# Kernel optimization log

Measured on AMD Instinct MI355X. Metric: run time of the kernel, lower is better.

The kernel has to match this reference:

```python
import jax, jax.numpy as jnp
import numpy as np

D_MODEL = 512; D_STATE = 64; D_CONV = 4; HEADDIM = 64
D_INNER = 2 * D_MODEL              # expand=2
NHEADS = D_INNER // HEADDIM        # 16
CONV_DIM = D_INNER + 2 * D_STATE   # 1152
D_IN_PROJ = 2 * D_INNER + 2 * D_STATE + NHEADS  # 2192
BATCH, SEQ = 4, 1024
EPS = 1e-5


def rmsnorm(x, w):
    return x * jax.lax.rsqrt(jnp.mean(x * x, axis=-1, keepdims=True) + EPS) * w


def mamba2(u, in_w, conv_w, conv_b, dt_bias, A_log, D, gnorm_w, out_w):
    b, l, _ = u.shape
    zxbcdt = u @ in_w.T                                  # [b,l,D_IN_PROJ]
    z = zxbcdt[..., :D_INNER]
    xBC = zxbcdt[..., D_INNER:D_INNER + CONV_DIM]
    dt = jax.nn.softplus(zxbcdt[..., -NHEADS:] + dt_bias)  # [b,l,h]
    # causal depthwise conv1d (kernel D_CONV, left pad) + silu
    pad = jnp.pad(xBC, ((0, 0), (D_CONV - 1, 0), (0, 0)))
    acc = conv_b
    for k in range(D_CONV):
        acc = acc + pad[:, k:k + l, :] * conv_w[:, k]
    xBC = jax.nn.silu(acc)
    x = xBC[..., :D_INNER].reshape(b, l, NHEADS, HEADDIM)
    Bm = xBC[..., D_INNER:D_INNER + D_STATE]             # [b,l,n]
    Cm = xBC[..., D_INNER + D_STATE:]                    # [b,l,n]
    A = -jnp.exp(A_log)                                  # [h]
    decay = jnp.exp(dt * A)                              # [b,l,h]
    dtx = dt[..., None] * x                              # [b,l,h,p]

    def step(h, inp):
        dec, dx, Bt, Ct = inp
        h = h * dec[:, :, None, None] + dx[..., None] * Bt[:, None, None, :]
        y = jnp.einsum('bhpn,bn->bhp', h, Ct)
        return h, y

    h0 = jnp.zeros((b, NHEADS, HEADDIM, D_STATE), u.dtype)
    _, ys = jax.lax.scan(step, h0, (decay.transpose(1, 0, 2),
                                    dtx.transpose(1, 0, 2, 3),
                                    Bm.transpose(1, 0, 2),
                                    Cm.transpose(1, 0, 2)))
    y = ys.transpose(1, 0, 2, 3) + x * D[None, None, :, None]  # [b,l,h,p]
    y = y.reshape(b, l, D_INNER)
    y = rmsnorm(y * jax.nn.silu(z), gnorm_w)             # gated RMSNorm
    return y @ out_w.T


def setup_inputs() -> dict:
    key = jax.random.key(0)
    ks = iter(jax.random.split(key, 32))
    def rn(shape, scale=0.02):
        return jax.random.normal(next(ks), shape, dtype=jnp.float32) * scale
    inp = {
        'x': jax.random.normal(next(ks), (BATCH, SEQ, D_MODEL), dtype=jnp.float32),
        'norm_w': jnp.ones((D_MODEL,), jnp.float32),
    }
    for p in ('f', 'b'):
        inp[p + '_in_w'] = rn((D_IN_PROJ, D_MODEL))
        inp[p + '_conv_w'] = rn((CONV_DIM, D_CONV), 0.1)
        inp[p + '_conv_b'] = jnp.zeros((CONV_DIM,), jnp.float32)
        inp[p + '_dt_bias'] = rn((NHEADS,), 0.5)
        inp[p + '_A_log'] = jnp.log(jnp.arange(1, NHEADS + 1, dtype=jnp.float32))
        inp[p + '_D'] = jnp.ones((NHEADS,), jnp.float32)
        inp[p + '_gnorm_w'] = jnp.ones((D_INNER,), jnp.float32)
        inp[p + '_out_w'] = rn((D_MODEL, D_INNER))
    inp['proj_w'] = rn((D_MODEL, 2 * D_MODEL))
    return inp


def reference(x, norm_w,
              f_in_w, f_conv_w, f_conv_b, f_dt_bias, f_A_log, f_D, f_gnorm_w, f_out_w,
              b_in_w, b_conv_w, b_conv_b, b_dt_bias, b_A_log, b_D, b_gnorm_w, b_out_w,
              proj_w):
    h = rmsnorm(x, norm_w)
    fo = mamba2(h, f_in_w, f_conv_w, f_conv_b, f_dt_bias, f_A_log, f_D, f_gnorm_w, f_out_w)
    bo = jnp.flip(mamba2(jnp.flip(h, 1), b_in_w, b_conv_w, b_conv_b, b_dt_bias,
                         b_A_log, b_D, b_gnorm_w, b_out_w), 1)
    return x + jnp.concatenate([fo, bo], axis=-1) @ proj_w.T
```

## Files before the change

### kernel.cpp

```cpp
#include <hip/hip_runtime.h>
#include <math.h>

typedef unsigned short u16;
typedef __bf16  bf16x8 __attribute__((ext_vector_type(8)));
typedef float   f32x4  __attribute__((ext_vector_type(4)));
typedef unsigned short u16x8 __attribute__((ext_vector_type(8)));

#define SEQ 1024
#define MR  4096
#define DIP 2192
#define DI  1024
#define NH  16
#define CD  1152
#define NCH 32
#define CT  32
#define NIN (DIP*512)
#define NOUT (512*1024)
#define ZROW 4384

__device__ __forceinline__ u16 f2bf(float f) {
  union { float f; unsigned u; } v; v.f = f;
  unsigned r = v.u + 0x7FFFu + ((v.u >> 16) & 1u);
  return (u16)(r >> 16);
}
__device__ __forceinline__ float bf2f(u16 h) {
  union { unsigned u; float f; } v; v.u = ((unsigned)h) << 16; return v.f;
}
__device__ __forceinline__ void splitbf(float v, u16& h, u16& l) {
  h = f2bf(v); l = f2bf(v - bf2f(h));
}
__device__ __forceinline__ float sigm(float x){ return 1.f/(1.f+__expf(-x)); }

__device__ __forceinline__ unsigned packbf(float v) {
  u16 hh, ll; splitbf(v, hh, ll);
  return (unsigned)hh | ((unsigned)ll << 16);
}
__device__ __forceinline__ float unpackf(unsigned w) {
  return bf2f((u16)w) + bf2f((u16)(w >> 16));
}

__device__ __forceinline__ void unpack8(const unsigned* p, bf16x8& H, bf16x8& L) {
  uint4 a = *(const uint4*)p, b = *(const uint4*)(p+4);
  u16x8 hu, lu;
  hu[0]=(u16)a.x; lu[0]=(u16)(a.x>>16);
  hu[1]=(u16)a.y; lu[1]=(u16)(a.y>>16);
  hu[2]=(u16)a.z; lu[2]=(u16)(a.z>>16);
  hu[3]=(u16)a.w; lu[3]=(u16)(a.w>>16);
  hu[4]=(u16)b.x; lu[4]=(u16)(b.x>>16);
  hu[5]=(u16)b.y; lu[5]=(u16)(b.y>>16);
  hu[6]=(u16)b.z; lu[6]=(u16)(b.z>>16);
  hu[7]=(u16)b.w; lu[7]=(u16)(b.w>>16);
  H = __builtin_bit_cast(bf16x8, hu);
  L = __builtin_bit_cast(bf16x8, lu);
}
__device__ __forceinline__ void unpack8s(const unsigned* p, int stride, bf16x8& H, bf16x8& L) {
  u16x8 hu, lu;
  #pragma unroll
  for (int jj=0;jj<8;jj++){ unsigned w = p[(size_t)jj*stride]; hu[jj]=(u16)w; lu[jj]=(u16)(w>>16); }
  H = __builtin_bit_cast(bf16x8, hu);
  L = __builtin_bit_cast(bf16x8, lu);
}

__device__ __forceinline__ void gl16(const u16* g, u16* l) {
  __builtin_amdgcn_global_load_lds((const __attribute__((address_space(1))) void*)g,
                                   (__attribute__((address_space(3))) void*)l,
                                   16, 0, 0);
}

__global__ __launch_bounds__(256) void prep(
  const float* __restrict__ x, const float* __restrict__ norm_w,
  const float* __restrict__ f_in, const float* __restrict__ b_in,
  const float* __restrict__ f_out, const float* __restrict__ b_out,
  const float* __restrict__ proj,
  u16* __restrict__ H, u16* __restrict__ L, unsigned* __restrict__ wpk,
  u16* __restrict__ hbh, u16* __restrict__ hbl)
{
  int blk = blockIdx.x, tid = threadIdx.x;
  if (blk < MR) {
    int m = blk;
    const float* xr = x + (size_t)m*512;
    float2 v = *(const float2*)&xr[tid*2];
    float ss = v.x*v.x + v.y*v.y;
    #pragma unroll
    for (int off=32; off; off>>=1) ss += __shfl_xor(ss, off, 64);
    __shared__ float red[4];
    if ((tid&63)==0) red[tid>>6] = ss;
    __syncthreads();
    float total = red[0]+red[1]+red[2]+red[3];
    float rs = rsqrtf(total*(1.f/512.f) + 1e-5f);
    float2 w2 = *(const float2*)&norm_w[tid*2];
    u16 h0,l0,h1,l1;
    splitbf(v.x*rs*w2.x, h0, l0);
    splitbf(v.y*rs*w2.y, h1, l1);
    *(unsigned*)&hbh[(size_t)m*512 + tid*2] = (unsigned)h0 | ((unsigned)h1<<16);
    *(unsigned*)&hbl[(size_t)m*512 + tid*2] = (unsigned)l0 | ((unsigned)l1<<16);
  } else {
    int i = (blk - MR)*256 + tid;
    constexpr int TOT = 2*NIN + 3*NOUT;
    if (i >= TOT) return;
    float v;
    if (i < NIN)               v = f_in[i];
    else if (i < 2*NIN)        v = b_in[i-NIN];
    else if (i < 2*NIN+NOUT)   v = f_out[i-2*NIN];
    else if (i < 2*NIN+2*NOUT) v = b_out[i-2*NIN-NOUT];
    else                       v = proj[i-2*NIN-2*NOUT];
    if (i < 2*NIN) {
      u16 hh, ll; splitbf(v, hh, ll);
      H[i] = hh; L[i] = ll;
    } else {
      wpk[i - 2*NIN] = packbf(v);
    }
  }
}

__global__ __launch_bounds__(256) void gemm_in(
    const u16* __restrict__ Ah, const u16* __restrict__ Al,
    const u16* __restrict__ Wh, const u16* __restrict__ Wl,
    float* __restrict__ C0,
    const unsigned* __restrict__ wpk,
    u16* __restrict__ Wch, u16* __restrict__ Wcl)
{
  constexpr int K = 512;
  constexpr int N = DIP;
  __shared__ __align__(16) u16 sAh[128*32];
  __shared__ __align__(16) u16 sAl[128*32];
  __shared__ __align__(16) u16 sBh[128*32];
  __shared__ __align__(16) u16 sBl[128*32];
  const int tid = threadIdx.x;
  if (blockIdx.y >= 18) {
    int widx = (blockIdx.y - 18)*64 + blockIdx.x*2 + blockIdx.z;
    int d = widx & 1;
    int p0 = ((widx>>1)&7)*128;
    int o0 = (widx>>4)*64;
    int wv = tid>>6, lane = tid&63;
    int quad = lane>>4, l16 = lane&15;
    const unsigned* owp = wpk + (size_t)d*NOUT;
    const unsigned* pjp = wpk + 2*(size_t)NOUT;
    int pc = p0 + wv*32;
    f32x4 acc[4][2] = {};
    for (int kt=0; kt<512; kt+=32) {
      bf16x8 ahf[4], alf[4], bhf[2], blf[2];
      #pragma unroll
      for (int ia=0; ia<4; ia++)
        unpack8(pjp + (size_t)(o0 + 16*ia + l16)*1024 + d*512 + kt + quad*8, ahf[ia], alf[ia]);
      #pragma unroll
      for (int jb=0; jb<2; jb++)
        unpack8s(owp + (size_t)(kt + quad*8)*1024 + pc + 16*jb + l16, 1024, bhf[jb], blf[jb]);
      #pragma unroll
      for (int ia=0; ia<4; ia++)
        #pragma unroll
        for (int jb=0; jb<2; jb++) {
          f32x4 t = __builtin_amdgcn_mfma_f32_16x16x32_bf16(ahf[ia], blf[jb], acc[ia][jb], 0,0,0);
          t       = __builtin_amdgcn_mfma_f32_16x16x32_bf16(alf[ia], bhf[jb], t,           0,0,0);
          acc[ia][jb] = __builtin_amdgcn_mfma_f32_16x16x32_bf16(ahf[ia], bhf[jb], t,       0,0,0);
        }
    }
    #pragma unroll
    for (int ia=0; ia<4; ia++)
    #pragma unroll
    for (int jb=0; jb<2; jb++)
    #pragma unroll
    for (int r=0; r<4; r++) {
      int o = o0 + 16*ia + quad*4 + r;
      int p = pc + 16*jb + l16;
      u16 hh, ll; splitbf(acc[ia][jb][r], hh, ll);
      Wch[(size_t)d*NOUT + (size_t)o*1024 + p] = hh;
      Wcl[(size_t)d*NOUT + (size_t)o*1024 + p] = ll;
    }
    return;
  }
  const int dir = blockIdx.z;
  const int m0 = blockIdx.x * 128;
  const int n0 = blockIdx.y * 128;
  const int lane = tid & 63;
  const int wid  = tid >> 6;
  const u16* wh_p = Wh + (size_t)dir*NIN;
  const u16* wl_p = Wl + (size_t)dir*NIN;
  const int j0 = wid, j1 = wid + 4;
  const int cp = lane & 3;
  auto goff = [&](int j, bool isB)->size_t {
    int row = 16*j + (lane>>2);
    int s = (row>>1) & 3;
    int kc = (cp ^ s) * 8;
    int grow;
    if (!isB) {
      grow = m0 + row;
      if (dir) grow = (grow & ~1023) + (1023 - (grow & 1023));
    } else {
      grow = n0 + row;
      if (grow >= N) grow = N-1;
    }
    return (size_t)grow*K + kc;
  };
  const size_t a0 = goff(j0,false), a1 = goff(j1,false);
  const size_t b0 = goff(j0,true),  b1 = goff(j1,true);
  const int wm = (wid & 1) * 64;
  const int wn = (wid >> 1) * 64;
  const int quad = lane >> 4;
  const int l16  = lane & 15;
  const int qx = quad ^ ((l16>>1)&3);
  const int baseA = ((wm + l16)*4 + qx)*8;
  const int baseB = ((wn + l16)*4 + qx)*8;
  f32x4 acc[4][4] = {};
  for (int kt = 0; kt < K; kt += 32) {
    __syncthreads();
    gl16(Ah + a0 + kt, &sAh[j0*512]);  gl16(Ah + a1 + kt, &sAh[j1*512]);
    gl16(Al + a0 + kt, &sAl[j0*512]);  gl16(Al + a1 + kt, &sAl[j1*512]);
    gl16(wh_p + b0 + kt, &sBh[j0*512]);  gl16(wh_p + b1 + kt, &sBh[j1*512]);
    gl16(wl_p + b0 + kt, &sBl[j0*512]);  gl16(wl_p + b1 + kt, &sBl[j1*512]);
    __syncthreads();
    bf16x8 ah[4], al[4], bh[4], bl[4];
    #pragma unroll
    for (int i=0;i<4;i++) {
      ah[i] = *(const bf16x8*)&sAh[baseA + i*512];
      al[i] = *(const bf16x8*)&sAl[baseA + i*512];
    }
    #pragma unroll
    for (int j=0;j<4;j++) {
      bh[j] = *(const bf16x8*)&sBh[baseB + j*512];
      bl[j] = *(const bf16x8*)&sBl[baseB + j*512];
    }
    #pragma unroll
    for (int i=0;i<4;i++)
      #pragma unroll
      for (int j=0;j<4;j++) {
        f32x4 t = __builtin_amdgcn_mfma_f32_16x16x32_bf16(ah[i], bl[j], acc[i][j], 0,0,0);
        t       = __builtin_amdgcn_mfma_f32_16x16x32_bf16(al[i], bh[j], t,         0,0,0);
        acc[i][j] = __builtin_amdgcn_mfma_f32_16x16x32_bf16(ah[i], bh[j], t,       0,0,0);
      }
  }
  #pragma unroll
  for (int i=0;i<4;i++)
  #pragma unroll
  for (int j=0;j<4;j++)
  #pragma unroll
  for (int r=0;r<4;r++) {
    int mo = m0 + wm + i*16 + quad*4 + r;
    int no = n0 + wn + j*16 + l16;
    if (no < N) C0[((size_t)dir*MR + mo)*DIP + no] = acc[i][j][r];
  }
}

__global__ __launch_bounds__(256) void gemm_final(
    const u16* __restrict__ zt, const u16* __restrict__ Wch, const u16* __restrict__ Wcl,
    const float* __restrict__ X0, float* __restrict__ out, float* __restrict__ Pb)
{
  constexpr int K = 1024;
  __shared__ __align__(16) u16 sAh[64*32];
  __shared__ __align__(16) u16 sAl[64*32];
  __shared__ __align__(16) u16 sBh[128*32];
  __shared__ __align__(16) u16 sBl[128*32];
  const int tid = threadIdx.x;
  const int dir = blockIdx.z;
  const int m0 = blockIdx.x * 64;
  const int n0 = blockIdx.y * 128;
  const int lane = tid & 63;
  const int wid  = tid >> 6;
  const u16* ah_p = zt + 2048 + (size_t)dir*MR*ZROW;
  const u16* al_p = zt + 3072 + (size_t)dir*MR*ZROW;
  const u16* wh_p = Wch + (size_t)dir*NOUT;
  const u16* wl_p = Wcl + (size_t)dir*NOUT;
  const int cp = lane & 3;
  auto goffA = [&](int j)->size_t {
    int row = 16*j + (lane>>2);
    int s = (row>>1) & 3;
    int kc = (cp ^ s) * 8;
    int grow = m0 + row;
    if (dir) grow = (grow & ~1023) + (1023 - (grow & 1023));
    return (size_t)grow*ZROW + kc;
  };
  auto goffB = [&](int j)->size_t {
    int row = 16*j + (lane>>2);
    int s = (row>>1) & 3;
    int kc = (cp ^ s) * 8;
    return (size_t)(n0 + row)*1024 + kc;
  };
  const size_t a0 = goffA(wid);
  const size_t b0 = goffB(wid), b1 = goffB(wid+4);
  const int quad = lane >> 4;
  const int l16  = lane & 15;
  const int qx = quad ^ ((l16>>1)&3);
  const int baseA = (l16*4 + qx)*8;
  const int baseB = ((wid*32 + l16)*4 + qx)*8;
  f32x4 acc[4][2] = {};
  for (int kt = 0; kt < K; kt += 32) {
    __syncthreads();
    gl16(ah_p + a0 + kt, &sAh[wid*512]);
    gl16(al_p + a0 + kt, &sAl[wid*512]);
    gl16(wh_p + b0 + kt, &sBh[wid*512]);  gl16(wh_p + b1 + kt, &sBh[(wid+4)*512]);
    gl16(wl_p + b0 + kt, &sBl[wid*512]);  gl16(wl_p + b1 + kt, &sBl[(wid+4)*512]);
    __syncthreads();
    bf16x8 ah[4], al[4], bh[2], bl[2];
    #pragma unroll
    for (int i=0;i<4;i++) {
      ah[i] = *(const bf16x8*)&sAh[baseA + i*512];
      al[i] = *(const bf16x8*)&sAl[baseA + i*512];
    }
    #pragma unroll
    for (int j=0;j<2;j++) {
      bh[j] = *(const bf16x8*)&sBh[baseB + j*512];
      bl[j] = *(const bf16x8*)&sBl[baseB + j*512];
    }
    #pragma unroll
    for (int i=0;i<4;i++)
      #pragma unroll
      for (int j=0;j<2;j++) {
        f32x4 t = __builtin_amdgcn_mfma_f32_16x16x32_bf16(ah[i], bl[j], acc[i][j], 0,0,0);
        t       = __builtin_amdgcn_mfma_f32_16x16x32_bf16(al[i], bh[j], t,         0,0,0);
        acc[i][j] = __builtin_amdgcn_mfma_f32_16x16x32_bf16(ah[i], bh[j], t,       0,0,0);
      }
  }
  #pragma unroll
  for (int i=0;i<4;i++)
  #pragma unroll
  for (int j=0;j<2;j++)
  #pragma unroll
  for (int r=0;r<4;r++) {
    int mo = m0 + i*16 + quad*4 + r;
    int no = n0 + wid*32 + j*16 + l16;
    float v = acc[i][j][r];
    if (dir == 0) out[(size_t)mo*512 + no] = v + X0[(size_t)mo*512 + no];
    else          Pb[(size_t)mo*512 + no] = v;
  }
}

__global__ __launch_bounds__(256) void addout(float* __restrict__ out,
                                              const float* __restrict__ Pb)
{
  size_t i = ((size_t)blockIdx.x*256 + threadIdx.x)*4;
  float4 a = *(const float4*)&out[i];
  float4 b = *(const float4*)&Pb[i];
  a.x += b.x; a.y += b.y; a.z += b.z; a.w += b.w;
  *(float4*)&out[i] = a;
}

__global__ __launch_bounds__(320) void conv_dt(
  const float* __restrict__ Z,
  const float* __restrict__ f_cw, const float* __restrict__ f_cb,
  const float* __restrict__ b_cw, const float* __restrict__ b_cb,
  const float* __restrict__ f_dtb, const float* __restrict__ b_dtb,
  unsigned* __restrict__ xconv,
  unsigned* __restrict__ Bc, unsigned* __restrict__ Cc,
  float* __restrict__ dtq)
{
  int bsw = blockIdx.x;
  int b = (bsw & 7)*256 + (bsw >> 3);
  int r0 = b*4;
  int dir = r0 >> 12;
  int t0 = r0 & 1023;
  const float* cw  = dir ? b_cw : f_cw;
  const float* cb  = dir ? b_cb : f_cb;
  const float* dtb = dir ? b_dtb : f_dtb;
  int tid = threadIdx.x;
  if (tid < 288) {
    int c0 = tid*4;
    float4 w0 = *(const float4*)&cw[c0*4];
    float4 w1 = *(const float4*)&cw[(c0+1)*4];
    float4 w2 = *(const float4*)&cw[(c0+2)*4];
    float4 w3 = *(const float4*)&cw[(c0+3)*4];
    float4 cb4 = *(const float4*)&cb[c0];
    const float4 zero4 = {0.f,0.f,0.f,0.f};
    float4 wnd[7];
    #pragma unroll
    for (int j=0;j<7;j++) {
      int a = r0 - 3 + j;
      wnd[j] = (a >= 0) ? *(const float4*)(Z + (size_t)a*DIP + 1024 + c0) : zero4;
    }
    #pragma unroll
    for (int k=0;k<4;k++) {
      int t = t0 + k;
      float4 z0 = (t >= 3) ? wnd[k]   : zero4;
      float4 z1 = (t >= 2) ? wnd[k+1] : zero4;
      float4 z2 = (t >= 1) ? wnd[k+2] : zero4;
      float4 z3 = wnd[k+3];
      float4 a = cb4;
      a.x += z0.x*w0.x + z1.x*w0.y + z2.x*w0.z + z3.x*w0.w;
      a.y += z0.y*w1.x + z1.y*w1.y + z2.y*w1.z + z3.y*w1.w;
      a.z += z0.z*w2.x + z1.z*w2.y + z2.z*w2.z + z3.z*w2.w;
      a.w += z0.w*w3.x + z1.w*w3.y + z2.w*w3.z + z3.w*w3.w;
      float4 v;
      v.x = a.x * sigm(a.x); v.y = a.y * sigm(a.y);
      v.z = a.z * sigm(a.z); v.w = a.w * sigm(a.w);
      uint4 pv;
      pv.x = packbf(v.x); pv.y = packbf(v.y);
      pv.z = packbf(v.z); pv.w = packbf(v.w);
      int bm = r0 + k;
      if (c0 < 1024)      *(uint4*)&xconv[(size_t)bm*DI + c0] = pv;
      else if (c0 < 1088) *(uint4*)&Bc[(size_t)bm*64 + (c0-1024)] = pv;
      else                *(uint4*)&Cc[(size_t)bm*64 + (c0-1088)] = pv;
    }
  }
  if (tid < NH) {
    #pragma unroll
    for (int k=0;k<4;k++) {
      int bm = r0 + k;
      float dtraw = Z[(size_t)bm*DIP + 2176 + tid] + dtb[tid];
      float dt = (dtraw > 20.f) ? dtraw : log1pf(__expf(dtraw));
      dtq[(size_t)bm*NH + tid] = dt;
    }
  }
}

__global__ __launch_bounds__(256) void scan_mfma(
  const float* __restrict__ dtq, const unsigned* __restrict__ xconv,
  const unsigned* __restrict__ Bc, const unsigned* __restrict__ Cc,
  const float* __restrict__ f_Al, const float* __restrict__ b_Al,
  float* __restrict__ yraw, float* __restrict__ cumdec, float* __restrict__ S)
{
  __shared__ __align__(16) u16 sMh[4][32*40];
  __shared__ __align__(16) u16 sMl[4][32*40];
  __shared__ float scum[4][32];
  __shared__ float sdt[4][32];
  int bx = blockIdx.x;
  int hq = bx & 3, chunk = (bx>>2)&(NCH-1), dirb = bx>>7;
  int w = threadIdx.x >> 6, lane = threadIdx.x & 63;
  int h = hq*4 + w;
  int base_row = dirb*1024 + chunk*CT;
  const int quad = lane >> 4, l16 = lane & 15;
  const float* Al = (dirb >= 4) ? b_Al : f_Al;
  float A = -__expf(Al[h]);
  float dtl = 0.f, cum = 0.f;
  if (lane < 32) { dtl = dtq[(size_t)(base_row + lane)*16 + h]; cum = dtl; }
  #pragma unroll
  for (int off=1; off<32; off<<=1) {
    int src = (lane >= off) ? lane-off : lane;
    float o = __shfl(cum, src);
    if (lane >= off && lane < 32) cum += o;
  }
  if (lane < 32) {
    sdt[w][lane]  = dtl;
    scum[w][lane] = cum;
    cumdec[(size_t)(base_row + lane)*16 + h] = __expf(A*cum);
  }
  bf16x8 chf[2][2], clf[2][2], bhf[2][2], blf[2][2];
  #pragma unroll
  for (int i=0;i<2;i++)
  #pragma unroll
  for (int kk=0;kk<2;kk++) {
    unpack8(Cc + (size_t)(base_row + 16*i + l16)*64 + kk*32 + quad*8, chf[i][kk], clf[i][kk]);
    unpack8(Bc + (size_t)(base_row + 16*i + l16)*64 + kk*32 + quad*8, bhf[i][kk], blf[i][kk]);
  }
  f32x4 g[2][2];
  __builtin_amdgcn_s_setprio(1);
  #pragma unroll
  for (int i=0;i<2;i++)
  #pragma unroll
  for (int j=0;j<2;j++) {
    f32x4 acc = {};
    #pragma unroll
    for (int kk=0;kk<2;kk++) {
      acc = __builtin_amdgcn_mfma_f32_16x16x32_bf16(chf[i][kk], blf[j][kk], acc, 0,0,0);
      acc = __builtin_amdgcn_mfma_f32_16x16x32_bf16(clf[i][kk], bhf[j][kk], acc, 0,0,0);
      acc = __builtin_amdgcn_mfma_f32_16x16x32_bf16(chf[i][kk], bhf[j][kk], acc, 0,0,0);
    }
    g[i][j] = acc;
  }
  __builtin_amdgcn_s_setprio(0);
  float ctt[2][4];
  #pragma unroll
  for (int i=0;i<2;i++)
  #pragma unroll
  for (int r=0;r<4;r++) ctt[i][r] = scum[w][16*i + quad*4 + r];
  #pragma unroll
  for (int j=0;j<2;j++) {
    int s = 16*j + l16;
    float cts = scum[w][s];
    float dts = sdt[w][s];
    #pragma unroll
    for (int i=0;i<2;i++)
    #pragma unroll
    for (int r=0;r<4;r++) {
      int t = 16*i + quad*4 + r;
      float mv = (s <= t) ? g[i][j][r] * __expf(A*(ctt[i][r]-cts)) * dts : 0.f;
      u16 hh, ll; splitbf(mv, hh, ll);
      sMh[w][t*40 + s] = hh;
      sMl[w][t*40 + s] = ll;
    }
  }
  bf16x8 xhf[4], xlf[4];
  const unsigned* xp = xconv + (size_t)(base_row + quad*8)*1024 + h*64 + l16;
  #pragma unroll
  for (int jp=0;jp<4;jp++) unpack8s(xp + 16*jp, 1024, xhf[jp], xlf[jp]);
  bf16x8 mhf[2], mlf[2];
  #pragma unroll
  for (int i=0;i<2;i++) {
    mhf[i] = *(const bf16x8*)&sMh[w][(16*i + l16)*40 + quad*8];
    mlf[i] = *(const bf16x8*)&sMl[w][(16*i + l16)*40 + quad*8];
  }
  __builtin_amdgcn_s_setprio(1);
  #pragma unroll
  for (int i=0;i<2;i++)
  #pragma unroll
  for (int jp=0;jp<4;jp++) {
    f32x4 acc = {};
    acc = __builtin_amdgcn_mfma_f32_16x16x32_bf16(mhf[i], xlf[jp], acc, 0,0,0);
    acc = __builtin_amdgcn_mfma_f32_16x16x32_bf16(mlf[i], xhf[jp], acc, 0,0,0);
    acc = __builtin_amdgcn_mfma_f32_16x16x32_bf16(mhf[i], xhf[jp], acc, 0,0,0);
    #pragma unroll
    for (int r=0;r<4;r++)
      yraw[(size_t)(base_row + 16*i + quad*4 + r)*1024 + h*64 + 16*jp + l16] = acc[r];
  }
  __builtin_amdgcn_s_setprio(0);
  float wv[8];
  float ct31 = scum[w][31];
  #pragma unroll
  for (int jj=0;jj<8;jj++) {
    int s = quad*8 + jj;
    wv[jj] = sdt[w][s] * __expf(A*(ct31 - scum[w][s]));
  }
  bf16x8 wbh[4], wbl[4];
  #pragma unroll
  for (int j2=0;j2<4;j2++) {
    u16x8 hu, lu; u16 hh, ll;
    #pragma unroll
    for (int jj=0;jj<8;jj++) {
      float b = unpackf(Bc[(size_t)(base_row + quad*8 + jj)*64 + 16*j2 + l16]);
      splitbf(wv[jj]*b, hh, ll); hu[jj]=hh; lu[jj]=ll;
    }
    wbh[j2] = __builtin_bit_cast(bf16x8, hu);
    wbl[j2] = __builtin_bit_cast(bf16x8, lu);
  }
  size_t inst = ((size_t)(dirb*16+h)*NCH + chunk)*4096;
  __builtin_amdgcn_s_setprio(1);
  #pragma unroll
  for (int mp=0;mp<4;mp++)
  #pragma unroll
  for (int j2=0;j2<4;j2++) {
    f32x4 acc = {};
    acc = __builtin_amdgcn_mfma_f32_16x16x32_bf16(xhf[mp], wbl[j2], acc, 0,0,0);
    acc = __builtin_amdgcn_mfma_f32_16x16x32_bf16(xlf[mp], wbh[j2], acc, 0,0,0);
    acc = __builtin_amdgcn_mfma_f32_16x16x32_bf16(xhf[mp], wbh[j2], acc, 0,0,0);
    #pragma unroll
    for (int r=0;r<4;r++)
      S[inst + (size_t)(16*mp + quad*4 + r)*64 + 16*j2 + l16] = acc[r];
  }
  __builtin_amdgcn_s_setprio(0);
}

__global__ __launch_bounds__(256) void scan_comb(
  const float* __restrict__ cumdec, float* __restrict__ S)
{
  int ih = blockIdx.x >> 4;
  int sub = blockIdx.x & 15;
  int dirb = ih >> 4, h = ih & 15;
  int elem = sub*256 + threadIdx.x;
  size_t base = (size_t)ih*NCH*4096 + elem;
  float hr = 0.f;
  #pragma unroll
  for (int c=0;c<NCH;c++) {
    float P = cumdec[((size_t)(dirb*1024 + c*CT + CT-1))*16 + h];
    float s = S[base + c*4096];
    S[base + c*4096] = __builtin_bit_cast(float, packbf(hr));
    hr = fmaf(hr, P, s);
  }
}

__global__ __launch_bounds__(1024) void scan_y2_gate(
  const unsigned* __restrict__ Cc, const float* __restrict__ cumdec,
  const float* __restrict__ S, const float* __restrict__ yraw,
  const unsigned* __restrict__ xconv, const float* Z, u16* zt,
  const float* __restrict__ f_D, const float* __restrict__ b_D,
  const float* __restrict__ f_gw, const float* __restrict__ b_gw)
{
  __shared__ float vbuf[32][1028];
  __shared__ float red[32][17];
  __shared__ float rsb[32];
  int bx = blockIdx.x;
  int chunk = bx & (NCH-1), dirb = bx >> 5;
  int w = threadIdx.x >> 6, lane = threadIdx.x & 63;
  int h = w;
  int dir = dirb >> 2;
  int row0 = dirb*1024 + chunk*CT;
  const int quad = lane>>4, l16 = lane&15;
  const float* Dp  = dir ? b_D  : f_D;
  const float* gwp = dir ? b_gw : f_gw;
  float Dv = Dp[h];

  f32x4 acc[2][4] = {};
  float at[2][4] = {};
  if (chunk > 0) {
    size_t inst = ((size_t)(dirb*16+h)*NCH + chunk)*4096;
    #pragma unroll
    for (int i=0;i<2;i++)
    #pragma unroll
    for (int r=0;r<4;r++)
      at[i][r] = cumdec[(size_t)(row0 + 16*i + quad*4 + r)*16 + h];
    bf16x8 chf[2][2], clf[2][2];
    #pragma unroll
    for (int i=0;i<2;i++)
    #pragma unroll
    for (int kk=0;kk<2;kk++)
      unpack8(Cc + (size_t)(row0 + 16*i + l16)*64 + kk*32 + quad*8, chf[i][kk], clf[i][kk]);
    const unsigned* Sp = (const unsigned*)S;
    __builtin_amdgcn_s_setprio(1);
    #pragma unroll
    for (int j=0;j<4;j++) {
      bf16x8 hhf[2], hlf[2];
      #pragma unroll
      for (int kk=0;kk<2;kk++)
        unpack8(Sp + inst + (size_t)(16*j + l16)*64 + kk*32 + quad*8, hhf[kk], hlf[kk]);
      #pragma unroll
      for (int i=0;i<2;i++) {
        f32x4 a2 = acc[i][j];
        #pragma unroll
        for (int kk=0;kk<2;kk++) {
          a2 = __builtin_amdgcn_mfma_f32_16x16x32_bf16(chf[i][kk], hlf[kk], a2, 0,0,0);
          a2 = __builtin_amdgcn_mfma_f32_16x16x32_bf16(clf[i][kk], hhf[kk], a2, 0,0,0);
          a2 = __builtin_amdgcn_mfma_f32_16x16x32_bf16(chf[i][kk], hhf[kk], a2, 0,0,0);
        }
        acc[i][j] = a2;
      }
    }
    __builtin_amdgcn_s_setprio(0);
  }
  float pss[2][4] = {};
  #pragma unroll
  for (int i=0;i<2;i++)
  #pragma unroll
  for (int r=0;r<4;r++) {
    int t = 16*i + quad*4 + r;
    size_t g = (size_t)(row0 + t);
    #pragma unroll
    for (int j=0;j<4;j++) {
      int c = h*64 + 16*j + l16;
      float yv = yraw[g*1024 + c];
      float xv = unpackf(xconv[g*1024 + c]);
      float zv = Z[g*DIP + c];
      float v = (yv + xv*Dv + at[i][r]*acc[i][j][r]) * (zv * sigm(zv));
      vbuf[t][c] = v;
      pss[i][r] += v*v;
    }
  }
  #pragma unroll
  for (int i=0;i<2;i++)
  #pragma unroll
  for (int r=0;r<4;r++) {
    float s2 = pss[i][r];
    s2 += __shfl_xor(s2, 1, 64);
    s2 += __shfl_xor(s2, 2, 64);
    s2 += __shfl_xor(s2, 4, 64);
    s2 += __shfl_xor(s2, 8, 64);
    if (l16 == 0) red[16*i + quad*4 + r][w] = s2;
  }
  __syncthreads();
  if (threadIdx.x < 32) {
    int t = threadIdx.x;
    float tot = 0.f;
    #pragma unroll
    for (int ww=0; ww<16; ww++) tot += red[t][ww];
    rsb[t] = rsqrtf(tot*(1.f/1024.f) + 1e-5f);
  }
  __syncthreads();
  #pragma unroll
  for (int i=0;i<2;i++)
  #pragma unroll
  for (int r=0;r<4;r++) {
    int t = 16*i + quad*4 + r;
    size_t g = (size_t)(row0 + t);
    float rs = rsb[t];
    #pragma unroll
    for (int j=0;j<4;j++) {
      int c = h*64 + 16*j + l16;
      float o = vbuf[t][c] * rs * gwp[c];
      u16 hh, ll; splitbf(o, hh, ll);
      zt[g*ZROW + 2048 + c] = hh;
      zt[g*ZROW + 3072 + c] = ll;
    }
  }
}

extern "C" void kernel_launch(void* const* d_in, const int* in_sizes, int n_in,
                              void* d_out, int out_size, void* d_ws, size_t ws_size,
                              hipStream_t stream)
{
  const float* x        = (const float*)d_in[0];
  const float* norm_w   = (const float*)d_in[1];
  const float* f_in_w   = (const float*)d_in[2];
  const float* f_conv_w = (const float*)d_in[3];
  const float* f_conv_b = (const float*)d_in[4];
  const float* f_dt_bias= (const float*)d_in[5];
  const float* f_A_log  = (const float*)d_in[6];
  const float* f_D      = (const float*)d_in[7];
  const float* f_gw     = (const float*)d_in[8];
  const float* f_out_w  = (const float*)d_in[9];
  const float* b_in_w   = (const float*)d_in[10];
  const float* b_conv_w = (const float*)d_in[11];
  const float* b_conv_b = (const float*)d_in[12];
  const float* b_dt_bias= (const float*)d_in[13];
  const float* b_A_log  = (const float*)d_in[14];
  const float* b_D      = (const float*)d_in[15];
  const float* b_gw     = (const float*)d_in[16];
  const float* b_out_w  = (const float*)d_in[17];
  const float* proj_w   = (const float*)d_in[18];

  char* ws = (char*)d_ws;
  size_t off = 0;
  auto alloc = [&](size_t bytes)->char* {
    char* p = ws + off; off = (off + bytes + 255) & ~(size_t)255; return p;
  };
  u16*   hbh   = (u16*)  alloc((size_t)MR*512*2);
  u16*   hbl   = (u16*)  alloc((size_t)MR*512*2);
  u16*   wH    = (u16*)  alloc(2*(size_t)NIN*2);
  u16*   wL    = (u16*)  alloc(2*(size_t)NIN*2);
  unsigned* wpk = (unsigned*)alloc(3*(size_t)NOUT*4);
  u16*   Wch   = (u16*)  alloc(2*(size_t)NOUT*2);
  u16*   Wcl   = (u16*)  alloc(2*(size_t)NOUT*2);
  float* Z     = (float*)alloc(2*(size_t)MR*DIP*4);
  unsigned* xconv = (unsigned*)alloc(2*(size_t)MR*DI*4);
  unsigned* Bc    = (unsigned*)alloc(2*(size_t)MR*64*4);
  unsigned* Cc    = (unsigned*)alloc(2*(size_t)MR*64*4);
  float* dtq   = (float*)alloc(2*(size_t)MR*NH*4);
  float* cumdec= (float*)alloc(2*(size_t)MR*NH*4);
  float* S     = (float*)alloc((size_t)4096*4096*4);
  float* yraw  = (float*)alloc(2*(size_t)MR*DI*4);
  u16* wih = wH;  u16* wil = wL;
  float* Pb = yraw;

  constexpr int TOT = 2*NIN + 3*NOUT;
  prep<<<MR + (TOT+255)/256,256,0,stream>>>(x, norm_w, f_in_w, b_in_w,
                                            f_out_w, b_out_w, proj_w,
                                            wH, wL, wpk, hbh, hbl);
  gemm_in<<<dim3(32,20,2),256,0,stream>>>(hbh, hbl, wih, wil, Z, wpk, Wch, Wcl);
  conv_dt<<<2048,320,0,stream>>>(Z, f_conv_w, f_conv_b, b_conv_w, b_conv_b,
                                 f_dt_bias, b_dt_bias, xconv, Bc, Cc, dtq);
  scan_mfma<<<1024,256,0,stream>>>(dtq, xconv, Bc, Cc, f_A_log, b_A_log,
                                   yraw, cumdec, S);
  scan_comb<<<2048,256,0,stream>>>(cumdec, S);
  scan_y2_gate<<<256,1024,0,stream>>>(Cc, cumdec, S, yraw, xconv, Z, (u16*)Z,
                                      f_D, b_D, f_gw, b_gw);
  gemm_final<<<dim3(64,4,2),256,0,stream>>>((u16*)Z, Wch, Wcl, x, (float*)d_out, Pb);
  addout<<<2048,256,0,stream>>>((float*)d_out, Pb);
}
```

Before: 347.3 us.

## Move intra-chunk scan output into the gate kernel and drop yraw round trip

The intra-chunk diagonal block (C·B^T mask times x) moves from scan_mfma into scan_y2_gate. The gate kernel recomputes the chunk cumsum of dt, accumulates the inter-chunk and intra-chunk contributions in registers, and keeps the gated values in registers rather than a large shared buffer. This removes the fp32 yraw write and re-read and the cumdec read. Separately, conv_dt now handles 8 rows per block, which halves the grid and cuts redundant window loads. In exchange the gate kernel does more MFMA work, more register work and more shared-memory staging per block, so occupancy may drop.

```diff
diff --git a/kernel.cpp b/kernel.cpp
--- a/kernel.cpp
+++ b/kernel.cpp
@@ -344,8 +344,8 @@
   float* __restrict__ dtq)
 {
   int bsw = blockIdx.x;
-  int b = (bsw & 7)*256 + (bsw >> 3);
-  int r0 = b*4;
+  int b = (bsw & 7)*128 + (bsw >> 3);
+  int r0 = b*8;
   int dir = r0 >> 12;
   int t0 = r0 & 1023;
   const float* cw  = dir ? b_cw : f_cw;
@@ -360,14 +360,14 @@
     float4 w3 = *(const float4*)&cw[(c0+3)*4];
     float4 cb4 = *(const float4*)&cb[c0];
     const float4 zero4 = {0.f,0.f,0.f,0.f};
-    float4 wnd[7];
-    #pragma unroll
-    for (int j=0;j<7;j++) {
+    float4 wnd[11];
+    #pragma unroll
+    for (int j=0;j<11;j++) {
       int a = r0 - 3 + j;
       wnd[j] = (a >= 0) ? *(const float4*)(Z + (size_t)a*DIP + 1024 + c0) : zero4;
     }
     #pragma unroll
-    for (int k=0;k<4;k++) {
+    for (int k=0;k<8;k++) {
       int t = t0 + k;
       float4 z0 = (t >= 3) ? wnd[k]   : zero4;
       float4 z1 = (t >= 2) ? wnd[k+1] : zero4;
@@ -392,7 +392,7 @@
   }
   if (tid < NH) {
     #pragma unroll
-    for (int k=0;k<4;k++) {
+    for (int k=0;k<8;k++) {
       int bm = r0 + k;
       float dtraw = Z[(size_t)bm*DIP + 2176 + tid] + dtb[tid];
       float dt = (dtraw > 20.f) ? dtraw : log1pf(__expf(dtraw));
@@ -403,12 +403,10 @@
 
 __global__ __launch_bounds__(256) void scan_mfma(
   const float* __restrict__ dtq, const unsigned* __restrict__ xconv,
-  const unsigned* __restrict__ Bc, const unsigned* __restrict__ Cc,
+  const unsigned* __restrict__ Bc,
   const float* __restrict__ f_Al, const float* __restrict__ b_Al,
-  float* __restrict__ yraw, float* __restrict__ cumdec, float* __restrict__ S)
-{
-  __shared__ __align__(16) u16 sMh[4][32*40];
-  __shared__ __align__(16) u16 sMl[4][32*40];
+  float* __restrict__ cumdec, float* __restrict__ S)
+{
   __shared__ float scum[4][32];
   __shared__ float sdt[4][32];
   int bx = blockIdx.x;
@@ -432,75 +430,10 @@
     scum[w][lane] = cum;
     cumdec[(size_t)(base_row + lane)*16 + h] = __expf(A*cum);
   }
-  bf16x8 chf[2][2], clf[2][2], bhf[2][2], blf[2][2];
-  #pragma unroll
-  for (int i=0;i<2;i++)
-  #pragma unroll
-  for (int kk=0;kk<2;kk++) {
-    unpack8(Cc + (size_t)(base_row + 16*i + l16)*64 + kk*32 + quad*8, chf[i][kk], clf[i][kk]);
-    unpack8(Bc + (size_t)(base_row + 16*i + l16)*64 + kk*32 + quad*8, bhf[i][kk], blf[i][kk]);
-  }
-  f32x4 g[2][2];
-  __builtin_amdgcn_s_setprio(1);
-  #pragma unroll
-  for (int i=0;i<2;i++)
-  #pragma unroll
-  for (int j=0;j<2;j++) {
-    f32x4 acc = {};
-    #pragma unroll
-    for (int kk=0;kk<2;kk++) {
-      acc = __builtin_amdgcn_mfma_f32_16x16x32_bf16(chf[i][kk], blf[j][kk], acc, 0,0,0);
-      acc = __builtin_amdgcn_mfma_f32_16x16x32_bf16(clf[i][kk], bhf[j][kk], acc, 0,0,0);
-      acc = __builtin_amdgcn_mfma_f32_16x16x32_bf16(chf[i][kk], bhf[j][kk], acc, 0,0,0);
-    }
-    g[i][j] = acc;
-  }
-  __builtin_amdgcn_s_setprio(0);
-  float ctt[2][4];
-  #pragma unroll
-  for (int i=0;i<2;i++)
-  #pragma unroll
-  for (int r=0;r<4;r++) ctt[i][r] = scum[w][16*i + quad*4 + r];
-  #pragma unroll
-  for (int j=0;j<2;j++) {
-    int s = 16*j + l16;
-    float cts = scum[w][s];
-    float dts = sdt[w][s];
-    #pragma unroll
-    for (int i=0;i<2;i++)
-    #pragma unroll
-    for (int r=0;r<4;r++) {
-      int t = 16*i + quad*4 + r;
-      float mv = (s <= t) ? g[i][j][r] * __expf(A*(ctt[i][r]-cts)) * dts : 0.f;
-      u16 hh, ll; splitbf(mv, hh, ll);
-      sMh[w][t*40 + s] = hh;
-      sMl[w][t*40 + s] = ll;
-    }
-  }
   bf16x8 xhf[4], xlf[4];
   const unsigned* xp = xconv + (size_t)(base_row + quad*8)*1024 + h*64 + l16;
   #pragma unroll
   for (int jp=0;jp<4;jp++) unpack8s(xp + 16*jp, 1024, xhf[jp], xlf[jp]);
-  bf16x8 mhf[2], mlf[2];
-  #pragma unroll
-  for (int i=0;i<2;i++) {
-    mhf[i] = *(const bf16x8*)&sMh[w][(16*i + l16)*40 + quad*8];
-    mlf[i] = *(const bf16x8*)&sMl[w][(16*i + l16)*40 + quad*8];
-  }
-  __builtin_amdgcn_s_setprio(1);
-  #pragma unroll
-  for (int i=0;i<2;i++)
-  #pragma unroll
-  for (int jp=0;jp<4;jp++) {
-    f32x4 acc = {};
-    acc = __builtin_amdgcn_mfma_f32_16x16x32_bf16(mhf[i], xlf[jp], acc, 0,0,0);
-    acc = __builtin_amdgcn_mfma_f32_16x16x32_bf16(mlf[i], xhf[jp], acc, 0,0,0);
-    acc = __builtin_amdgcn_mfma_f32_16x16x32_bf16(mhf[i], xhf[jp], acc, 0,0,0);
-    #pragma unroll
-    for (int r=0;r<4;r++)
-      yraw[(size_t)(base_row + 16*i + quad*4 + r)*1024 + h*64 + 16*jp + l16] = acc[r];
-  }
-  __builtin_amdgcn_s_setprio(0);
   float wv[8];
   float ct31 = scum[w][31];
   #pragma unroll
@@ -556,13 +489,17 @@
 }
 
 __global__ __launch_bounds__(1024) void scan_y2_gate(
-  const unsigned* __restrict__ Cc, const float* __restrict__ cumdec,
-  const float* __restrict__ S, const float* __restrict__ yraw,
-  const unsigned* __restrict__ xconv, const float* Z, u16* zt,
+  const unsigned* __restrict__ Cc, const unsigned* __restrict__ Bc,
+  const float* __restrict__ S, const unsigned* __restrict__ xconv,
+  const float* Z, u16* zt, const float* __restrict__ dtq,
+  const float* __restrict__ f_Al, const float* __restrict__ b_Al,
   const float* __restrict__ f_D, const float* __restrict__ b_D,
   const float* __restrict__ f_gw, const float* __restrict__ b_gw)
 {
-  __shared__ float vbuf[32][1028];
+  __shared__ __align__(16) u16 sMh[16][32*40];
+  __shared__ __align__(16) u16 sMl[16][32*40];
+  __shared__ float sdt2[16][32];
+  __shared__ float scum2[16][32];
   __shared__ float red[32][17];
   __shared__ float rsb[32];
   int bx = blockIdx.x;
@@ -572,25 +509,76 @@
   int dir = dirb >> 2;
   int row0 = dirb*1024 + chunk*CT;
   const int quad = lane>>4, l16 = lane&15;
+  const float* Alp = (dirb >= 4) ? b_Al : f_Al;
   const float* Dp  = dir ? b_D  : f_D;
   const float* gwp = dir ? b_gw : f_gw;
+  float A = -__expf(Alp[h]);
   float Dv = Dp[h];
-
+  float dtl = 0.f, cum = 0.f;
+  if (lane < 32) { dtl = dtq[(size_t)(row0 + lane)*16 + h]; cum = dtl; }
+  #pragma unroll
+  for (int off=1; off<32; off<<=1) {
+    int src = (lane >= off) ? lane-off : lane;
+    float o = __shfl(cum, src);
+    if (lane >= off && lane < 32) cum += o;
+  }
+  if (lane < 32) { sdt2[h][lane] = dtl; scum2[h][lane] = cum; }
+  bf16x8 chf[2][2], clf[2][2];
+  f32x4 g[2][2];
+  {
+    bf16x8 bhf[2][2], blf[2][2];
+    #pragma unroll
+    for (int i=0;i<2;i++)
+    #pragma unroll
+    for (int kk=0;kk<2;kk++) {
+      unpack8(Cc + (size_t)(row0 + 16*i + l16)*64 + kk*32 + quad*8, chf[i][kk], clf[i][kk]);
+      unpack8(Bc + (size_t)(row0 + 16*i + l16)*64 + kk*32 + quad*8, bhf[i][kk], blf[i][kk]);
+    }
+    __builtin_amdgcn_s_setprio(1);
+    #pragma unroll
+    for (int i=0;i<2;i++)
+    #pragma unroll
+    for (int j=0;j<2;j++) {
+      f32x4 acc = {};
+      #pragma unroll
+      for (int kk=0;kk<2;kk++) {
+        acc = __builtin_amdgcn_mfma_f32_16x16x32_bf16(chf[i][kk], blf[j][kk], acc, 0,0,0);
+        acc = __builtin_amdgcn_mfma_f32_16x16x32_bf16(clf[i][kk], bhf[j][kk], acc, 0,0,0);
+        acc = __builtin_amdgcn_mfma_f32_16x16x32_bf16(chf[i][kk], bhf[j][kk], acc, 0,0,0);
+      }
+      g[i][j] = acc;
+    }
+    __builtin_amdgcn_s_setprio(0);
+  }
+  float ctt[2][4];
+  #pragma unroll
+  for (int i=0;i<2;i++)
+  #pragma unroll
+  for (int r=0;r<4;r++) ctt[i][r] = scum2[h][16*i + quad*4 + r];
+  #pragma unroll
+  for (int j=0;j<2;j++) {
+    int s = 16*j + l16;
+    float cts = scum2[h][s];
+    float dts = sdt2[h][s];
+    #pragma unroll
+    for (int i=0;i<2;i++)
+    #pragma unroll
+    for (int r=0;r<4;r++) {
+      int t = 16*i + quad*4 + r;
+      float mv = (s <= t) ? g[i][j][r] * __expf(A*(ctt[i][r]-cts)) * dts : 0.f;
+      u16 hh, ll; splitbf(mv, hh, ll);
+      sMh[h][t*40 + s] = hh;
+      sMl[h][t*40 + s] = ll;
+    }
+  }
+  float at[2][4];
+  #pragma unroll
+  for (int i=0;i<2;i++)
+  #pragma unroll
+  for (int r=0;r<4;r++) at[i][r] = __expf(A*ctt[i][r]);
   f32x4 acc[2][4] = {};
-  float at[2][4] = {};
   if (chunk > 0) {
     size_t inst = ((size_t)(dirb*16+h)*NCH + chunk)*4096;
-    #pragma unroll
-    for (int i=0;i<2;i++)
-    #pragma unroll
-    for (int r=0;r<4;r++)
-      at[i][r] = cumdec[(size_t)(row0 + 16*i + quad*4 + r)*16 + h];
-    bf16x8 chf[2][2], clf[2][2];
-    #pragma unroll
-    for (int i=0;i<2;i++)
-    #pragma unroll
-    for (int kk=0;kk<2;kk++)
-      unpack8(Cc + (size_t)(row0 + 16*i + l16)*64 + kk*32 + quad*8, chf[i][kk], clf[i][kk]);
     const unsigned* Sp = (const unsigned*)S;
     __builtin_amdgcn_s_setprio(1);
     #pragma unroll
@@ -601,15 +589,40 @@
         unpack8(Sp + inst + (size_t)(16*j + l16)*64 + kk*32 + quad*8, hhf[kk], hlf[kk]);
       #pragma unroll
       for (int i=0;i<2;i++) {
-        f32x4 a2 = acc[i][j];
+        f32x4 a2 = {};
         #pragma unroll
         for (int kk=0;kk<2;kk++) {
           a2 = __builtin_amdgcn_mfma_f32_16x16x32_bf16(chf[i][kk], hlf[kk], a2, 0,0,0);
           a2 = __builtin_amdgcn_mfma_f32_16x16x32_bf16(clf[i][kk], hhf[kk], a2, 0,0,0);
           a2 = __builtin_amdgcn_mfma_f32_16x16x32_bf16(chf[i][kk], hhf[kk], a2, 0,0,0);
         }
-        acc[i][j] = a2;
+        #pragma unroll
+        for (int r=0;r<4;r++) acc[i][j][r] = at[i][r]*a2[r];
       }
+    }
+    __builtin_amdgcn_s_setprio(0);
+  }
+  {
+    bf16x8 xhf[4], xlf[4];
+    const unsigned* xp = xconv + (size_t)(row0 + quad*8)*1024 + h*64 + l16;
+    #pragma unroll
+    for (int jp=0;jp<4;jp++) unpack8s(xp + 16*jp, 1024, xhf[jp], xlf[jp]);
+    bf16x8 mhf[2], mlf[2];
+    #pragma unroll
+    for (int i=0;i<2;i++) {
+      mhf[i] = *(const bf16x8*)&sMh[h][(16*i + l16)*40 + quad*8];
+      mlf[i] = *(const bf16x8*)&sMl[h][(16*i + l16)*40 + quad*8];
+    }
+    __builtin_amdgcn_s_setprio(1);
+    #pragma unroll
+    for (int i=0;i<2;i++)
+    #pragma unroll
+    for (int jp=0;jp<4;jp++) {
+      f32x4 a2 = acc[i][jp];
+      a2 = __builtin_amdgcn_mfma_f32_16x16x32_bf16(mhf[i], xlf[jp], a2, 0,0,0);
+      a2 = __builtin_amdgcn_mfma_f32_16x16x32_bf16(mlf[i], xhf[jp], a2, 0,0,0);
+      a2 = __builtin_amdgcn_mfma_f32_16x16x32_bf16(mhf[i], xhf[jp], a2, 0,0,0);
+      acc[i][jp] = a2;
     }
     __builtin_amdgcn_s_setprio(0);
   }
@@ -619,15 +632,14 @@
   #pragma unroll
   for (int r=0;r<4;r++) {
     int t = 16*i + quad*4 + r;
-    size_t g = (size_t)(row0 + t);
+    size_t gg = (size_t)(row0 + t);
     #pragma unroll
     for (int j=0;j<4;j++) {
       int c = h*64 + 16*j + l16;
-      float yv = yraw[g*1024 + c];
-      float xv = unpackf(xconv[g*1024 + c]);
-      float zv = Z[g*DIP + c];
-      float v = (yv + xv*Dv + at[i][r]*acc[i][j][r]) * (zv * sigm(zv));
-      vbuf[t][c] = v;
+      float xv = unpackf(xconv[gg*1024 + c]);
+      float zv = Z[gg*DIP + c];
+      float v = (acc[i][j][r] + xv*Dv) * (zv * sigm(zv));
+      acc[i][j][r] = v;
       pss[i][r] += v*v;
     }
   }
@@ -656,15 +668,15 @@
   #pragma unroll
   for (int r=0;r<4;r++) {
     int t = 16*i + quad*4 + r;
-    size_t g = (size_t)(row0 + t);
+    size_t gg = (size_t)(row0 + t);
     float rs = rsb[t];
     #pragma unroll
     for (int j=0;j<4;j++) {
       int c = h*64 + 16*j + l16;
-      float o = vbuf[t][c] * rs * gwp[c];
+      float o = acc[i][j][r] * rs * gwp[c];
       u16 hh, ll; splitbf(o, hh, ll);
-      zt[g*ZROW + 2048 + c] = hh;
-      zt[g*ZROW + 3072 + c] = ll;
+      zt[gg*ZROW + 2048 + c] = hh;
+      zt[gg*ZROW + 3072 + c] = ll;
     }
   }
 }
@@ -721,13 +733,12 @@
                                             f_out_w, b_out_w, proj_w,
                                             wH, wL, wpk, hbh, hbl);
   gemm_in<<<dim3(32,20,2),256,0,stream>>>(hbh, hbl, wih, wil, Z, wpk, Wch, Wcl);
-  conv_dt<<<2048,320,0,stream>>>(Z, f_conv_w, f_conv_b, b_conv_w, b_conv_b,
+  conv_dt<<<1024,320,0,stream>>>(Z, f_conv_w, f_conv_b, b_conv_w, b_conv_b,
                                  f_dt_bias, b_dt_bias, xconv, Bc, Cc, dtq);
-  scan_mfma<<<1024,256,0,stream>>>(dtq, xconv, Bc, Cc, f_A_log, b_A_log,
-                                   yraw, cumdec, S);
+  scan_mfma<<<1024,256,0,stream>>>(dtq, xconv, Bc, f_A_log, b_A_log, cumdec, S);
   scan_comb<<<2048,256,0,stream>>>(cumdec, S);
-  scan_y2_gate<<<256,1024,0,stream>>>(Cc, cumdec, S, yraw, xconv, Z, (u16*)Z,
-                                      f_D, b_D, f_gw, b_gw);
+  scan_y2_gate<<<256,1024,0,stream>>>(Cc, Bc, S, xconv, Z, (u16*)Z, dtq,
+                                      f_A_log, b_A_log, f_D, b_D, f_gw, b_gw);
   gemm_final<<<dim3(64,4,2),256,0,stream>>>((u16*)Z, Wch, Wcl, x, (float*)d_out, Pb);
   addout<<<2048,256,0,stream>>>((float*)d_out, Pb);
 }
```

Result: no change. 342.4 us (-1.4%).
